# Kernel optimization log

Measured on AMD Instinct MI355X. Metric: run time of the kernel, lower is better.

The kernel has to match this reference:

```python
import jax, jax.numpy as jnp
import numpy as np

BS, FH, FW, NA = 32, 100, 100, 9
IMG_H, IMG_W = 1600, 1600
STRIDE = 16
KEEP_PRE, KEEP_POST, NMS_THR = 1000, 300, 0.7


def _grid_anchors():
    scales = np.array([128.0, 256.0, 512.0])
    ratios = np.array([0.5, 1.0, 2.0])
    ws, hs = [], []
    for s in scales:
        for r in ratios:
            ws.append(s * np.sqrt(1.0 / r))
            hs.append(s * np.sqrt(r))
    ws, hs = np.array(ws), np.array(hs)  # [9]
    sx = (np.arange(FW) + 0.5) * STRIDE
    sy = (np.arange(FH) + 0.5) * STRIDE
    cx, cy = np.meshgrid(sx, sy)  # [FH,FW]
    cx = cx.reshape(-1, 1)
    cy = cy.reshape(-1, 1)
    anchors = np.stack([
        cx - 0.5 * ws, cy - 0.5 * hs, cx + 0.5 * ws, cy + 0.5 * hs
    ], axis=-1).reshape(-1, 4)  # [FH*FW*NA, 4]
    return anchors.astype(np.float32)


def setup_inputs() -> dict:
    key = jax.random.key(0)
    k1, k2 = jax.random.split(key)
    N = FH * FW * NA
    cls_logits = jax.random.normal(k1, (BS, N, 1), dtype=jnp.float32)
    reg_deltas = jax.random.normal(k2, (BS, N, 4), dtype=jnp.float32) * 0.3
    anchors = jnp.asarray(_grid_anchors())
    return {"cls_logits": cls_logits, "reg_deltas": reg_deltas,
            "anchors": anchors, "img_h": IMG_H, "img_w": IMG_W}


def _offsets2boxes(deltas, anchors):
    # deltas: [bs,N,4] (dx,dy,dw,dh); anchors: [N,4] xyxy
    aw = anchors[:, 2] - anchors[:, 0]
    ah = anchors[:, 3] - anchors[:, 1]
    acx = anchors[:, 0] + 0.5 * aw
    acy = anchors[:, 1] + 0.5 * ah
    cx = deltas[..., 0] * aw + acx
    cy = deltas[..., 1] * ah + acy
    w = jnp.exp(deltas[..., 2]) * aw
    h = jnp.exp(deltas[..., 3]) * ah
    return jnp.stack([cx - 0.5 * w, cy - 0.5 * h, cx + 0.5 * w, cy + 0.5 * h], axis=-1)


def _iou_matrix(b):
    # b: [K,4] -> [K,K]
    area = (b[:, 2] - b[:, 0]) * (b[:, 3] - b[:, 1])
    lt = jnp.maximum(b[:, None, :2], b[None, :, :2])
    rb = jnp.minimum(b[:, None, 2:], b[None, :, 2:])
    wh = jnp.clip(rb - lt, 0.0)
    inter = wh[..., 0] * wh[..., 1]
    return inter / (area[:, None] + area[None, :] - inter + 1e-12)


def _detect_single(boxes, scores, img_h, img_w):
    # boxes: [N,4], scores: [N]
    top_scores, idx = jax.lax.top_k(scores, KEEP_PRE)
    b = boxes[idx]  # [K,4], already score-sorted descending
    b = jnp.stack([
        jnp.clip(b[:, 0], 0.0, img_w), jnp.clip(b[:, 1], 0.0, img_h),
        jnp.clip(b[:, 2], 0.0, img_w), jnp.clip(b[:, 3], 0.0, img_h)
    ], axis=-1)
    iou = _iou_matrix(b)  # [K,K]
    K = KEEP_PRE
    cols = jnp.arange(K)

    def body(i, keep):
        # if box i still kept, suppress later boxes with IoU > thr (greedy NMS)
        sup = keep[i] & (iou[i] > NMS_THR) & (cols > i)
        return keep & ~sup

    keep = jax.lax.fori_loop(0, K, body, jnp.ones((K,), dtype=bool))
    # kept boxes first (stable sort preserves descending-score order), take top P
    order = jnp.argsort(~keep, stable=True)[:KEEP_POST]
    valid = keep[order]
    det = jnp.concatenate([b[order], top_scores[order, None]], axis=-1)
    return det * valid[:, None].astype(det.dtype)  # padded rows zeroed


def reference(cls_logits, reg_deltas, anchors, img_h, img_w):
    bs = cls_logits.shape[0]
    scores = jax.nn.sigmoid(cls_logits.reshape(bs, -1))  # [bs,N]
    boxes = _offsets2boxes(reg_deltas.reshape(bs, -1, 4), anchors)  # [bs,N,4]
    fh = jnp.float32(img_h)
    fw = jnp.float32(img_w)
    dets = jax.vmap(lambda b, s: _detect_single(b, s, fh, fw))(boxes, scores)
    return dets  # [bs, KEEP_POST, 5] (xmin,ymin,xmax,ymax,score), zero-padded
```

## Files before the change

kernel.cpp:

```cpp
#include <hip/hip_runtime.h>
#include <stdint.h>

#pragma clang fp contract(off)

#define BS 32
#define NANCH 90000
#define KEEP_PRE 1000
#define KEEP_POST 300
#define NMS_THR 0.7f
#define NBINS 4096
#define HREP 4129
#define CAND_MAX 4096
#define MW 16
#define CNT_STRIDE 32
#define NSLICE 8
#define NF4 22500

typedef unsigned long long u64;
typedef unsigned int u32;

#define CNT_OFF    0
#define CNT_BYTES  ((size_t)BS * CNT_STRIDE * 4)
#define CAND_OFF   (CNT_OFF + CNT_BYTES)
#define BOX_OFF    (CAND_OFF + (size_t)BS * CAND_MAX * 8)
#define SCORE_OFF  (BOX_OFF + (size_t)BS * KEEP_PRE * 16)
#define MASK_OFF   (SCORE_OFF + (size_t)BS * KEEP_PRE * 4)

__device__ __forceinline__ u32 fmono(float f) {
    u32 u = __float_as_uint(f);
    return (u & 0x80000000u) ? ~u : (u | 0x80000000u);
}

__global__ __launch_bounds__(1024) void prep_kernel(const float* __restrict__ logits,
                                                    u32* __restrict__ cnt,
                                                    u64* __restrict__ cand) {
    __shared__ u32 lh[2][HREP];
    __shared__ u32 parts[1024];
    __shared__ u32 s_B;
    __shared__ u32 s_cnt;
    const int b = blockIdx.x;
    const int tid = threadIdx.x;
    u32* h0 = lh[0];
    u32* h1 = lh[1];

    for (int i = tid; i < 2 * HREP; i += 1024) ((u32*)lh)[i] = 0;
    if (tid == 0) s_cnt = 0;
    __syncthreads();

    const float4* src4 = (const float4*)(logits + (size_t)b * NANCH);
    u32* myh = lh[tid & 1];

#define H1_(f) do { u32 m_ = fmono(f); atomicAdd(&myh[m_ >> 20], 1u); } while (0)
#define HIST4_(v) do { H1_((v).x); H1_((v).y); H1_((v).z); H1_((v).w); } while (0)

    for (int j = 0; j < 20; j += 4) {
        float4 va = src4[tid + (j + 0) * 1024];
        float4 vb = src4[tid + (j + 1) * 1024];
        float4 vc = src4[tid + (j + 2) * 1024];
        float4 vd = src4[tid + (j + 3) * 1024];
        HIST4_(va); HIST4_(vb); HIST4_(vc); HIST4_(vd);
    }
    {
        float4 ve = src4[tid + 20 * 1024];
        HIST4_(ve);
        if (tid < NF4 - 21 * 1024) {
            float4 vf = src4[tid + 21 * 1024];
            HIST4_(vf);
        }
    }
    __syncthreads();

    {
        int g = tid * 4;
        parts[tid] = h0[g] + h1[g] + h0[g + 1] + h1[g + 1]
                   + h0[g + 2] + h1[g + 2] + h0[g + 3] + h1[g + 3];
    }
    __syncthreads();
    if (tid < 64) {
        u32 g64 = 0;
#pragma unroll
        for (int k = 0; k < 16; k++) g64 += parts[tid * 16 + k];
        u32 s = g64;
#pragma unroll
        for (int off = 1; off < 64; off <<= 1) {
            u32 x = __shfl_down(s, off);
            if (tid + off < 64) s += x;
        }
        if (s >= KEEP_PRE && (s - g64) < KEEP_PRE) {
            u32 cum = s - g64;
            int stop = tid * 64;
            int bin = stop + 63;
            u32 B = (u32)stop;
            for (; bin >= stop; bin--) {
                u32 hb = h0[bin] + h1[bin];
                if (cum + hb >= KEEP_PRE) { B = (u32)bin; break; }
                cum += hb;
            }
            s_B = B;
        }
    }
    __syncthreads();
    const u32 B = s_B;

    const u32 lane = tid & 63;
    u64* dst = cand + (size_t)b * CAND_MAX;
    for (int j = 0; j < 22; ++j) {
        int idx4 = tid + (j << 10);
        bool inb = idx4 < NF4;
        float4 v = make_float4(0.f, 0.f, 0.f, 0.f);
        if (inb) v = src4[idx4];
        u32 mm[4];
        mm[0] = fmono(v.x); mm[1] = fmono(v.y); mm[2] = fmono(v.z); mm[3] = fmono(v.w);
#pragma unroll
        for (int k = 0; k < 4; k++) {
            bool is = inb && ((mm[k] >> 20) >= B);
            u64 bal = __ballot(is);
            if (bal) {
                u32 old = 0;
                if (lane == 0) old = atomicAdd(&s_cnt, (u32)__popcll(bal));
                u32 wbase = __shfl(old, 0);
                if (is) {
                    u32 prefix = (u32)__popcll(bal & ((1ull << lane) - 1ull));
                    u32 pos = wbase + prefix;
                    u32 i = (u32)(idx4 * 4 + k);
                    if (pos < CAND_MAX)
                        dst[pos] = ((u64)mm[k] << 32) | (u32)(~i);
                }
            }
        }
    }
    __syncthreads();
    if (tid == 0) cnt[b * CNT_STRIDE] = s_cnt;
#undef H1_
#undef HIST4_
}

__global__ __launch_bounds__(256) void select_kernel(const float* __restrict__ deltas,
                                                     const float* __restrict__ anchors,
                                                     const u32* __restrict__ cnt,
                                                     const u64* __restrict__ cand,
                                                     float4* __restrict__ selbox,
                                                     float* __restrict__ selscore,
                                                     const int* __restrict__ p_img_h,
                                                     const int* __restrict__ p_img_w) {
    __shared__ u64 keys[CAND_MAX];
    const int b = blockIdx.y;
    const int slice = blockIdx.x;
    const int n = (int)min(cnt[b * CNT_STRIDE], (u32)CAND_MAX);
    const u64* src = cand + (size_t)b * CAND_MAX;
    for (int i = threadIdx.x; i < n; i += 256)
        keys[i] = src[i];
    __syncthreads();
    const int per = (n + NSLICE - 1) / NSLICE;
    const int i0 = slice * per;
    const int i1 = min(i0 + per, n);
    const float W = (float)(*p_img_w);
    const float H = (float)(*p_img_h);
    const float4* d4 = (const float4*)deltas;
    const float4* a4 = (const float4*)anchors;
    for (int i = i0 + threadIdx.x; i < i1; i += 256) {
        const u64 me = keys[i];
        int rank = 0;
        int j = 0;
        for (; j + 16 <= n; j += 16) {
            int r0 = 0;
#pragma unroll
            for (int k = 0; k < 16; k++) r0 += (keys[j + k] > me);
            rank += r0;
        }
        for (; j < n; j++) rank += (keys[j] > me);
        if (rank < KEEP_PRE) {
            u32 idx = ~(u32)me;
            u32 m = (u32)(me >> 32);
            u32 ub = (m & 0x80000000u) ? (m ^ 0x80000000u) : ~m;
            float logit = __uint_as_float(ub);
            float score = 1.0f / (1.0f + expf(-logit));
            float4 d = d4[(size_t)b * NANCH + idx];
            float4 a = a4[idx];
            float aw = a.z - a.x, ah = a.w - a.y;
            float acx = a.x + 0.5f * aw, acy = a.y + 0.5f * ah;
            float cx = d.x * aw + acx, cy = d.y * ah + acy;
            float w = expf(d.z) * aw, h = expf(d.w) * ah;
            float x1 = cx - 0.5f * w, y1 = cy - 0.5f * h;
            float x2 = cx + 0.5f * w, y2 = cy + 0.5f * h;
            x1 = fminf(fmaxf(x1, 0.0f), W); y1 = fminf(fmaxf(y1, 0.0f), H);
            x2 = fminf(fmaxf(x2, 0.0f), W); y2 = fminf(fmaxf(y2, 0.0f), H);
            selbox[(size_t)b * KEEP_PRE + rank] = make_float4(x1, y1, x2, y2);
            selscore[(size_t)b * KEEP_PRE + rank] = score;
        }
    }
}

__global__ __launch_bounds__(256) void iou_kernel(const float4* __restrict__ selbox,
                                                  u64* __restrict__ mask) {
    const int b = blockIdx.y;
    const int bx = blockIdx.x;
    int c, w;
    if (bx < 16)      { c = 0; w = bx; }
    else if (bx < 28) { c = 1; w = bx - 12; }
    else if (bx < 36) { c = 2; w = bx - 20; }
    else              { c = 3; w = bx - 24; }
    const int i = c * 256 + threadIdx.x;
    __shared__ float4 cb[64];
    __shared__ float ca[64];
    if (threadIdx.x < 64) {
        int j = w * 64 + threadIdx.x;
        float4 bx4 = (j < KEEP_PRE) ? selbox[(size_t)b * KEEP_PRE + j]
                                    : make_float4(0, 0, 0, 0);
        cb[threadIdx.x] = bx4;
        ca[threadIdx.x] = (bx4.z - bx4.x) * (bx4.w - bx4.y);
    }
    __syncthreads();
    if (i >= KEEP_PRE) return;
    float4 bi = selbox[(size_t)b * KEEP_PRE + i];
    float ai = (bi.z - bi.x) * (bi.w - bi.y);
    const int jbase = w * 64;
    u64 bits = 0;
#pragma unroll 8
    for (int jj = 0; jj < 64; jj++) {
        float4 bj = cb[jj];
        float ltx = fmaxf(bi.x, bj.x), lty = fmaxf(bi.y, bj.y);
        float rbx = fminf(bi.z, bj.z), rby = fminf(bi.w, bj.w);
        float wx = fmaxf(rbx - ltx, 0.0f), wy = fmaxf(rby - lty, 0.0f);
        float inter = wx * wy;
        float denom = ai + ca[jj] - inter + 1e-12f;
        if (inter / denom > NMS_THR) bits |= (1ull << jj);
    }
    int lo = i + 1 - jbase;
    u64 mlo = (lo <= 0) ? ~0ull : ((lo >= 64) ? 0ull : (~0ull << lo));
    int hi = KEEP_PRE - jbase;
    u64 mhi = (hi >= 64) ? ~0ull : ((1ull << hi) - 1ull);
    mask[((size_t)b * KEEP_PRE + i) * MW + w] = bits & mlo & mhi;
}

#define CH_ROWS 64
#define CH_WORDS (CH_ROWS * MW)
#define NCHUNK ((KEEP_PRE + CH_ROWS - 1) / CH_ROWS)

__global__ __launch_bounds__(256) void nms_out_kernel(const u64* __restrict__ mask,
                                                      const float4* __restrict__ selbox,
                                                      const float* __restrict__ selscore,
                                                      float* __restrict__ out) {
    const int b = blockIdx.x;
    __shared__ u64 lbuf[2][CH_WORDS];
    __shared__ u64 keepw[MW];
    __shared__ u32 wpre[MW + 1];
    __shared__ int ls_stop;
    const int tid = threadIdx.x;
    const u64* mrow = mask + (size_t)b * KEEP_PRE * MW;

    auto load_chunk = [&](int c) {
        int idx = tid - 128;
        if (idx < 0) return;
        const int words = (c == NCHUNK - 1)
                            ? (KEEP_PRE - (NCHUNK - 1) * CH_ROWS) * MW
                            : CH_WORDS;
        const u64* gsrc = mrow + (size_t)c * CH_WORDS;
        u64* dst = lbuf[c & 1];
#pragma unroll
        for (int k = 0; k < 4; k++) {
            int off = k * 256 + idx * 2;
            ulonglong2 v;
            if (off < words) v = *(const ulonglong2*)(gsrc + off);
            else { v.x = 0ull; v.y = 0ull; }
            *(ulonglong2*)(dst + off) = v;
        }
    };

    if (tid == 0) ls_stop = 0;
    load_chunk(0);
    __syncthreads();

    u64 remv = 0;
    int kept_total = 0;
    const int lw = tid & 15;
    for (int c = 0; c < NCHUNK; c++) {
        if (c + 1 < NCHUNK) load_chunk(c + 1);
        if (tid < 64) {
            const u64* lb = lbuf[c & 1];
            const int wmin = (c >> 2) << 2;
            const u64 vmask = (lw >= wmin) ? ~0ull : 0ull;
            u64 cur = __shfl(remv, c);
#pragma unroll
            for (int blk = 0; blk < 8; blk++) {
                u64 R[8], rwv[8];
#pragma unroll
                for (int k = 0; k < 8; k++)
                    R[k] = lb[(size_t)(blk * 8 + k) * MW + lw] & vmask;
#pragma unroll
                for (int k = 0; k < 8; k++)
                    rwv[k] = lb[(size_t)(blk * 8 + k) * MW + c];
#pragma unroll
                for (int k = 0; k < 8; k++) {
                    const int p = blk * 8 + k;
                    u64 msk = ((cur >> p) & 1ull) ? 0ull : ~0ull;
                    remv |= R[k] & msk;
                    cur  |= rwv[k] & msk;
                }
            }
            kept_total += 64 - (int)__popcll(cur);
            if (c + 1 < NCHUNK && kept_total >= KEEP_POST) {
                if (lw > c) remv = ~0ull;
                if (tid == 0) ls_stop = 1;
            }
        }
        __syncthreads();
        if (ls_stop) break;
    }

    if (tid < MW) {
        u64 kw = ~remv;
        if (tid == MW - 1) kw &= (1ull << (KEEP_PRE - 64 * (MW - 1))) - 1ull;
        keepw[tid] = kw;
    }
    __syncthreads();
    if (tid == 0) {
        u32 cnt = 0;
        for (int w = 0; w < MW; w++) { wpre[w] = cnt; cnt += (u32)__popcll(keepw[w]); }
        wpre[MW] = cnt;
    }
    __syncthreads();
    const int total = (int)wpre[MW];
    float* outb = out + (size_t)b * KEEP_POST * 5;
    for (int i = tid; i < KEEP_PRE; i += 256) {
        int w = i >> 6;
        u64 kw = keepw[w];
        if ((kw >> (i & 63)) & 1ull) {
            int rank = (int)wpre[w] + __popcll(kw & ((1ull << (i & 63)) - 1ull));
            if (rank < KEEP_POST) {
                float4 bx = selbox[(size_t)b * KEEP_PRE + i];
                float sc = selscore[(size_t)b * KEEP_PRE + i];
                outb[rank * 5 + 0] = bx.x;
                outb[rank * 5 + 1] = bx.y;
                outb[rank * 5 + 2] = bx.z;
                outb[rank * 5 + 3] = bx.w;
                outb[rank * 5 + 4] = sc;
            }
        }
    }
    for (int r = tid; r < KEEP_POST; r += 256) {
        if (r >= total) {
            outb[r * 5 + 0] = 0.0f;
            outb[r * 5 + 1] = 0.0f;
            outb[r * 5 + 2] = 0.0f;
            outb[r * 5 + 3] = 0.0f;
            outb[r * 5 + 4] = 0.0f;
        }
    }
}

extern "C" void kernel_launch(void* const* d_in, const int* in_sizes, int n_in,
                              void* d_out, int out_size, void* d_ws, size_t ws_size,
                              hipStream_t stream) {
    const float* logits  = (const float*)d_in[0];
    const float* deltas  = (const float*)d_in[1];
    const float* anchors = (const float*)d_in[2];
    const int* p_img_h   = (const int*)d_in[3];
    const int* p_img_w   = (const int*)d_in[4];

    char* ws = (char*)d_ws;
    u32* cnt       = (u32*)(ws + CNT_OFF);
    u64* cand      = (u64*)(ws + CAND_OFF);
    float4* selbox = (float4*)(ws + BOX_OFF);
    float* selscore = (float*)(ws + SCORE_OFF);
    u64* mask      = (u64*)(ws + MASK_OFF);

    prep_kernel<<<dim3(BS), 1024, 0, stream>>>(logits, cnt, cand);
    select_kernel<<<dim3(NSLICE, BS), 256, 0, stream>>>(deltas, anchors, cnt, cand,
                                                        selbox, selscore, p_img_h, p_img_w);
    iou_kernel<<<dim3(40, BS), 256, 0, stream>>>(selbox, mask);
    nms_out_kernel<<<BS, 256, 0, stream>>>(mask, selbox, selscore, (float*)d_out);
}
```

Before: 178.0 us.

## Fuse top-k selection into prep kernel with bin-bucketed candidate ranking

Merges the candidate-selection kernel into the histogram kernel. A full prefix scan over the histogram bins scatters candidates into shared memory grouped by bin, so each candidate's rank comes from comparisons within its own bin plus a bin offset, instead of against all candidates. This drops a kernel launch, the global round trip for the candidate list, and most of the quadratic rank comparisons. In exchange the selection work runs on only 32 blocks instead of 256, and it uses more shared memory per block.

```diff
diff --git a/kernel.cpp b/kernel.cpp
--- a/kernel.cpp
+++ b/kernel.cpp
@@ -12,17 +12,12 @@
 #define HREP 4129
 #define CAND_MAX 4096
 #define MW 16
-#define CNT_STRIDE 32
-#define NSLICE 8
 #define NF4 22500
 
 typedef unsigned long long u64;
 typedef unsigned int u32;
 
-#define CNT_OFF    0
-#define CNT_BYTES  ((size_t)BS * CNT_STRIDE * 4)
-#define CAND_OFF   (CNT_OFF + CNT_BYTES)
-#define BOX_OFF    (CAND_OFF + (size_t)BS * CAND_MAX * 8)
+#define BOX_OFF    0
 #define SCORE_OFF  (BOX_OFF + (size_t)BS * KEEP_PRE * 16)
 #define MASK_OFF   (SCORE_OFF + (size_t)BS * KEEP_PRE * 4)
 
@@ -32,19 +27,25 @@
 }
 
 __global__ __launch_bounds__(1024) void prep_kernel(const float* __restrict__ logits,
-                                                    u32* __restrict__ cnt,
-                                                    u64* __restrict__ cand) {
+                                                    const float* __restrict__ deltas,
+                                                    const float* __restrict__ anchors,
+                                                    float4* __restrict__ selbox,
+                                                    float* __restrict__ selscore,
+                                                    const int* __restrict__ p_img_h,
+                                                    const int* __restrict__ p_img_w) {
     __shared__ u32 lh[2][HREP];
-    __shared__ u32 parts[1024];
+    __shared__ u32 S[NBINS + 1];
+    __shared__ u64 grp[CAND_MAX];
+    __shared__ u32 wtot[16], wexc[16];
     __shared__ u32 s_B;
-    __shared__ u32 s_cnt;
     const int b = blockIdx.x;
     const int tid = threadIdx.x;
+    const u32 lane = tid & 63;
+    const int wv = tid >> 6;
     u32* h0 = lh[0];
     u32* h1 = lh[1];
 
     for (int i = tid; i < 2 * HREP; i += 1024) ((u32*)lh)[i] = 0;
-    if (tid == 0) s_cnt = 0;
     __syncthreads();
 
     const float4* src4 = (const float4*)(logits + (size_t)b * NANCH);
@@ -70,105 +71,88 @@
     }
     __syncthreads();
 
+    const int g = tid * 4;
+    const u32 c0 = h0[g] + h1[g];
+    const u32 c1 = h0[g + 1] + h1[g + 1];
+    const u32 c2 = h0[g + 2] + h1[g + 2];
+    const u32 c3 = h0[g + 3] + h1[g + 3];
     {
-        int g = tid * 4;
-        parts[tid] = h0[g] + h1[g] + h0[g + 1] + h1[g + 1]
-                   + h0[g + 2] + h1[g + 2] + h0[g + 3] + h1[g + 3];
-    }
-    __syncthreads();
-    if (tid < 64) {
-        u32 g64 = 0;
-#pragma unroll
-        for (int k = 0; k < 16; k++) g64 += parts[tid * 16 + k];
-        u32 s = g64;
+        u32 s = c0 + c1 + c2 + c3;
 #pragma unroll
         for (int off = 1; off < 64; off <<= 1) {
             u32 x = __shfl_down(s, off);
-            if (tid + off < 64) s += x;
-        }
-        if (s >= KEEP_PRE && (s - g64) < KEEP_PRE) {
-            u32 cum = s - g64;
-            int stop = tid * 64;
-            int bin = stop + 63;
-            u32 B = (u32)stop;
-            for (; bin >= stop; bin--) {
-                u32 hb = h0[bin] + h1[bin];
-                if (cum + hb >= KEEP_PRE) { B = (u32)bin; break; }
-                cum += hb;
-            }
-            s_B = B;
-        }
+            if (lane + off < 64) s += x;
+        }
+        if (lane == 0) wtot[wv] = s;
+        __syncthreads();
+        if (tid < 16) {
+            u32 v = wtot[tid];
+            u32 t = v;
+#pragma unroll
+            for (int off = 1; off < 16; off <<= 1) {
+                u32 x = __shfl_down(t, off);
+                if (tid + off < 16) t += x;
+            }
+            wexc[tid] = t - v;
+        }
+        __syncthreads();
+        const u32 base = wexc[wv] + s;
+        S[g]     = base;
+        S[g + 1] = base - c0;
+        S[g + 2] = base - c0 - c1;
+        S[g + 3] = base - c0 - c1 - c2;
+        if (tid == 1023) S[NBINS] = 0;
+    }
+    __syncthreads();
+
+    {
+#pragma unroll
+        for (int k = 0; k < 4; k++) {
+            int bin = g + k;
+            if (S[bin] >= KEEP_PRE && S[bin + 1] < KEEP_PRE) s_B = (u32)bin;
+        }
+        h0[g] = 0; h0[g + 1] = 0; h0[g + 2] = 0; h0[g + 3] = 0;
     }
     __syncthreads();
     const u32 B = s_B;
-
-    const u32 lane = tid & 63;
-    u64* dst = cand + (size_t)b * CAND_MAX;
+    const int n_cap = (int)min(S[B], (u32)CAND_MAX);
+    u32* fill = h0;
+
     for (int j = 0; j < 22; ++j) {
         int idx4 = tid + (j << 10);
-        bool inb = idx4 < NF4;
-        float4 v = make_float4(0.f, 0.f, 0.f, 0.f);
-        if (inb) v = src4[idx4];
+        if (idx4 >= NF4) break;
+        float4 v = src4[idx4];
         u32 mm[4];
         mm[0] = fmono(v.x); mm[1] = fmono(v.y); mm[2] = fmono(v.z); mm[3] = fmono(v.w);
 #pragma unroll
         for (int k = 0; k < 4; k++) {
-            bool is = inb && ((mm[k] >> 20) >= B);
-            u64 bal = __ballot(is);
-            if (bal) {
-                u32 old = 0;
-                if (lane == 0) old = atomicAdd(&s_cnt, (u32)__popcll(bal));
-                u32 wbase = __shfl(old, 0);
-                if (is) {
-                    u32 prefix = (u32)__popcll(bal & ((1ull << lane) - 1ull));
-                    u32 pos = wbase + prefix;
-                    u32 i = (u32)(idx4 * 4 + k);
-                    if (pos < CAND_MAX)
-                        dst[pos] = ((u64)mm[k] << 32) | (u32)(~i);
-                }
-            }
-        }
-    }
-    __syncthreads();
-    if (tid == 0) cnt[b * CNT_STRIDE] = s_cnt;
-#undef H1_
-#undef HIST4_
-}
-
-__global__ __launch_bounds__(256) void select_kernel(const float* __restrict__ deltas,
-                                                     const float* __restrict__ anchors,
-                                                     const u32* __restrict__ cnt,
-                                                     const u64* __restrict__ cand,
-                                                     float4* __restrict__ selbox,
-                                                     float* __restrict__ selscore,
-                                                     const int* __restrict__ p_img_h,
-                                                     const int* __restrict__ p_img_w) {
-    __shared__ u64 keys[CAND_MAX];
-    const int b = blockIdx.y;
-    const int slice = blockIdx.x;
-    const int n = (int)min(cnt[b * CNT_STRIDE], (u32)CAND_MAX);
-    const u64* src = cand + (size_t)b * CAND_MAX;
-    for (int i = threadIdx.x; i < n; i += 256)
-        keys[i] = src[i];
-    __syncthreads();
-    const int per = (n + NSLICE - 1) / NSLICE;
-    const int i0 = slice * per;
-    const int i1 = min(i0 + per, n);
+            u32 bin = mm[k] >> 20;
+            if (bin >= B) {
+                u32 pos = S[bin + 1] + atomicAdd(&fill[bin], 1u);
+                u32 i = (u32)(idx4 * 4 + k);
+                if (pos < (u32)CAND_MAX)
+                    grp[pos] = ((u64)mm[k] << 32) | (u32)(~i);
+            }
+        }
+    }
+    __syncthreads();
+
     const float W = (float)(*p_img_w);
     const float H = (float)(*p_img_h);
     const float4* d4 = (const float4*)deltas;
     const float4* a4 = (const float4*)anchors;
-    for (int i = i0 + threadIdx.x; i < i1; i += 256) {
-        const u64 me = keys[i];
-        int rank = 0;
-        int j = 0;
-        for (; j + 16 <= n; j += 16) {
-            int r0 = 0;
-#pragma unroll
-            for (int k = 0; k < 16; k++) r0 += (keys[j + k] > me);
-            rank += r0;
-        }
-        for (; j < n; j++) rank += (keys[j] > me);
+    for (int p = tid; p < n_cap; p += 1024) {
+        const u64 me = grp[p];
+        const int bin = (int)(me >> 52);
+        const int gb = (int)S[bin + 1];
+        const int ge = min((int)S[bin], n_cap);
+        int rank = gb;
+        int q = gb;
+        for (; q + 4 <= ge; q += 4) {
+            rank += (grp[q] > me) + (grp[q + 1] > me)
+                  + (grp[q + 2] > me) + (grp[q + 3] > me);
+        }
+        for (; q < ge; q++) rank += (grp[q] > me);
         if (rank < KEEP_PRE) {
             u32 idx = ~(u32)me;
             u32 m = (u32)(me >> 32);
@@ -189,6 +173,8 @@
             selscore[(size_t)b * KEEP_PRE + rank] = score;
         }
     }
+#undef H1_
+#undef HIST4_
 }
 
 __global__ __launch_bounds__(256) void iou_kernel(const float4* __restrict__ selbox,
@@ -359,15 +345,12 @@
     const int* p_img_w   = (const int*)d_in[4];
 
     char* ws = (char*)d_ws;
-    u32* cnt       = (u32*)(ws + CNT_OFF);
-    u64* cand      = (u64*)(ws + CAND_OFF);
-    float4* selbox = (float4*)(ws + BOX_OFF);
+    float4* selbox  = (float4*)(ws + BOX_OFF);
     float* selscore = (float*)(ws + SCORE_OFF);
-    u64* mask      = (u64*)(ws + MASK_OFF);
-
-    prep_kernel<<<dim3(BS), 1024, 0, stream>>>(logits, cnt, cand);
-    select_kernel<<<dim3(NSLICE, BS), 256, 0, stream>>>(deltas, anchors, cnt, cand,
-                                                        selbox, selscore, p_img_h, p_img_w);
+    u64* mask       = (u64*)(ws + MASK_OFF);
+
+    prep_kernel<<<dim3(BS), 1024, 0, stream>>>(logits, deltas, anchors,
+                                               selbox, selscore, p_img_h, p_img_w);
     iou_kernel<<<dim3(40, BS), 256, 0, stream>>>(selbox, mask);
     nms_out_kernel<<<BS, 256, 0, stream>>>(mask, selbox, selscore, (float*)d_out);
 }
```

After: 170.3 us. 1.05x faster.
